# Performance work log

Hardware: AMD Instinct MI355X
Metric: run time of the kernel (lower is better)

Reference implementation:

```python
import jax, jax.numpy as jnp
import numpy as np

B, T, F, U, OUT_STEPS = 512, 128, 64, 1024, 24


def setup_inputs() -> dict:
    key = jax.random.key(0)
    k0, k1, k2, k3 = jax.random.split(key, 4)
    return {
        "inputs": jax.random.normal(k0, (B, T, F), jnp.float32),
        "Wx": jax.random.normal(k1, (F, 4 * U), jnp.float32) * 0.05,   # input kernel, gates [i|f|g|o]
        "Wh": jax.random.normal(k2, (U, 4 * U), jnp.float32) * 0.02,   # recurrent kernel
        "b": jnp.zeros((4 * U,), jnp.float32),
        "Wd": jax.random.normal(k3, (U, F), jnp.float32) * 0.03,       # Dense readout
        "bd": jnp.zeros((F,), jnp.float32),
    }


def _lstm_step(h, c, x, Wx, Wh, b):
    # Keras LSTMCell: gate order i, f, g(candidate), o; sigmoid recurrent act, tanh act.
    z = x @ Wx + h @ Wh + b                      # [B, 4U]
    i, f, g, o = jnp.split(z, 4, axis=-1)
    i = jax.nn.sigmoid(i)
    f = jax.nn.sigmoid(f)
    g = jnp.tanh(g)
    o = jax.nn.sigmoid(o)
    c_new = f * c + i * g
    h_new = o * jnp.tanh(c_new)
    return h_new, c_new


def reference(inputs, Wx, Wh, b, Wd, bd):
    Bq = inputs.shape[0]
    Uq = Wh.shape[0]
    h0 = jnp.zeros((Bq, Uq), inputs.dtype)
    c0 = jnp.zeros((Bq, Uq), inputs.dtype)

    # ---- warmup: run full LSTM over the input window, keep final state ----
    def warm(carry, x_t):
        h, c = carry
        h, c = _lstm_step(h, c, x_t, Wx, Wh, b)
        return (h, c), None

    (h, c), _ = jax.lax.scan(warm, (h0, c0), jnp.swapaxes(inputs, 0, 1))  # scan over time
    pred = h @ Wd + bd                            # first prediction [B, F]

    def decode(carry, _):
        h, c, p = carry
        h, c = _lstm_step(h, c, p, Wx, Wh, b)
        p = h @ Wd + bd
        return (h, c, p), p

    _, rest = jax.lax.scan(decode, (h, c, pred), None, length=OUT_STEPS - 1)
    preds = jnp.concatenate([pred[None], rest], axis=0)   # [OUT_STEPS, B, F]
    return jnp.swapaxes(preds, 0, 1)                       # [B, OUT_STEPS, F]
```

## Files before the change

kernel.cpp:

```cpp
#include <hip/hip_runtime.h>
#include <math.h>

#define Bq 512
#define Tq 128
#define Fq 64
#define Uq 1024
#define OSTEPS 24
#define NKC16 68

typedef _Float16 f16x8 __attribute__((ext_vector_type(8)));
typedef _Float16 f16x2 __attribute__((ext_vector_type(2)));
typedef float f32x16 __attribute__((ext_vector_type(16)));
typedef float f32x4 __attribute__((ext_vector_type(4)));
typedef float f32x2 __attribute__((ext_vector_type(2)));

__device__ __forceinline__ float sigmoidf_(float x) {
    return 1.0f / (1.0f + __expf(-x));
}
__device__ __forceinline__ float tanhf_(float x) {
    return 2.0f / (1.0f + __expf(-2.0f * x)) - 1.0f;
}

#define BAR() do {                                             \
    asm volatile("s_waitcnt lgkmcnt(0)" ::: "memory");         \
    __builtin_amdgcn_s_barrier();                              \
} while (0)

__global__ __launch_bounds__(256)
void pack_w(const float* __restrict__ Wh, const float* __restrict__ Wx,
            f16x8* __restrict__ BpH)
{
    long id = (long)blockIdx.x * 256 + threadIdx.x;
    int lane = (int)(id & 63);
    long rest = id >> 6;
    int kc16 = (int)(rest % NKC16);
    int gcol = (int)(rest / NKC16);
    int col = (gcol >> 5) * Uq + (gcol & 31) * 32 + (lane & 31);
    int k0 = kc16 * 16 + (lane >> 5) * 8;
    f16x8 hv;
#pragma unroll
    for (int j = 0; j < 8; ++j) {
        int k = k0 + j;
        float v = (k < Uq) ? Wh[(size_t)k * (4 * Uq) + col]
                           : Wx[(size_t)(k - Uq) * (4 * Uq) + col];
        hv[j] = (_Float16)v;
    }
    BpH[id] = hv;
}

#define STAGE_LOAD4(wl, bank) do {                                              \
    _Pragma("unroll")                                                           \
    for (int j_ = 0; j_ < 4; ++j_)                                              \
        ash[bank][j_] = *(const f16x8*)(hrow + ((wl) * 4 + j_) * 64);           \
} while (0)

#define STAGE_WRITE4(buf, bank) do {                                            \
    _Pragma("unroll")                                                           \
    for (int j_ = 0; j_ < 4; ++j_)                                              \
        As[buf][j_][smh][sslot] = ash[bank][j_];                                \
} while (0)

#define LOADB4(slot, wl) do {                                                   \
    _Pragma("unroll")                                                           \
    for (int j_ = 0; j_ < 4; ++j_) {                                            \
        Bh[slot][j_][0] = bpH0[(((wl) * 4 + j_) * 4 + kq) * 64];                \
        Bh[slot][j_][1] = bpH1[(((wl) * 4 + j_) * 4 + kq) * 64];                \
    }                                                                           \
} while (0)

#define COMPUTE4(buf, slot) do {                                                \
    _Pragma("unroll")                                                           \
    for (int j_ = 0; j_ < 4; ++j_) {                                            \
        f16x8 ah0_ = As[buf][j_][0][rdslot];                                    \
        f16x8 ah1_ = As[buf][j_][1][rdslot];                                    \
        __builtin_amdgcn_s_setprio(1);                                          \
        acc[0][0] = __builtin_amdgcn_mfma_f32_32x32x16_f16(ah0_, Bh[slot][j_][0], acc[0][0], 0, 0, 0); \
        acc[0][1] = __builtin_amdgcn_mfma_f32_32x32x16_f16(ah1_, Bh[slot][j_][0], acc[0][1], 0, 0, 0); \
        acc[1][0] = __builtin_amdgcn_mfma_f32_32x32x16_f16(ah0_, Bh[slot][j_][1], acc[1][0], 0, 0, 0); \
        acc[1][1] = __builtin_amdgcn_mfma_f32_32x32x16_f16(ah1_, Bh[slot][j_][1], acc[1][1], 0, 0, 0); \
        __builtin_amdgcn_s_setprio(0);                                          \
    }                                                                           \
} while (0)

__global__ __launch_bounds__(512, 2)
void lstm_step(const _Float16* __restrict__ h_in,
               const float* __restrict__ xsrc,
               long xstride,
               const f16x8* __restrict__ BpH,
               const float* __restrict__ bias,
               _Float16* __restrict__ h_out,
               float* __restrict__ c_st)
{
    __shared__ __align__(16) char smem[73728];
    f16x8 (*As)[4][2][256] = (f16x8 (*)[4][2][256])smem;
    f16x8 (*xbuf)[256] = (f16x8 (*)[256])(smem + 65536);
    float (*zsd)[4][32][36] = (float (*)[4][32][36])smem;

    const int tid = threadIdx.x;
    const int l   = tid & 63;
    const int w   = tid >> 6;
    const int gp  = w & 1;
    const int kq  = w >> 1;
    const int bm  = (int)blockIdx.x >> 5;
    const int bu  = (int)blockIdx.x & 31;
    const int row0 = bm * 64;

    const int srow = tid >> 3;
    const int kg8  = tid & 7;
    const int smh  = srow >> 5;
    const int sr31 = srow & 31;
    const int sslot = sr31 * 8 + (kg8 ^ (sr31 & 7));

    const int rdslot = (l & 31) * 8 + ((kq * 2 + (l >> 5)) ^ (l & 7));

    const f16x8* bpH0 = BpH + ((size_t)((gp * 2 + 0) * 32 + bu) * NKC16) * 64 + l;
    const f16x8* bpH1 = BpH + ((size_t)((gp * 2 + 1) * 32 + bu) * NKC16) * 64 + l;
    const _Float16* hrow = h_in + (size_t)(row0 + srow) * Uq + kg8 * 8;
    const float*    xrow = xsrc + (size_t)(row0 + srow) * xstride + kg8 * 8;

    f32x16 acc[2][2];
#pragma unroll
    for (int i = 0; i < 16; ++i) {
        acc[0][0][i] = 0.0f; acc[0][1][i] = 0.0f;
        acc[1][0][i] = 0.0f; acc[1][1][i] = 0.0f;
    }

    f16x8 Bh[2][4][2];
    f16x8 Bx[2];
    f16x8 ash[2][4];

    {
        f32x4 v0_ = *(const f32x4*)xrow;
        f32x4 v1_ = *(const f32x4*)(xrow + 4);
        f16x8 hv_;
#pragma unroll
        for (int j_ = 0; j_ < 4; ++j_) {
            hv_[j_]     = (_Float16)v0_[j_];
            hv_[4 + j_] = (_Float16)v1_[j_];
        }
        xbuf[smh][sslot] = hv_;
    }
    Bx[0] = bpH0[(64 + kq) * 64];
    Bx[1] = bpH1[(64 + kq) * 64];
    STAGE_LOAD4(0, 0);
    STAGE_LOAD4(1, 1);
    LOADB4(0, 0);
    STAGE_WRITE4(0, 0);
    BAR();

    LOADB4(1, 1);
    STAGE_LOAD4(2, 0);
    STAGE_WRITE4(1, 1);
    COMPUTE4(0, 0);
    BAR();
    LOADB4(0, 2);
    STAGE_LOAD4(3, 1);
    STAGE_WRITE4(0, 0);
    COMPUTE4(1, 1);
    BAR();
    LOADB4(1, 3);
    STAGE_WRITE4(1, 1);
    COMPUTE4(0, 0);
    BAR();
    COMPUTE4(1, 1);
    {
        f16x8 ah0_ = xbuf[0][rdslot];
        f16x8 ah1_ = xbuf[1][rdslot];
        acc[0][0] = __builtin_amdgcn_mfma_f32_32x32x16_f16(ah0_, Bx[0], acc[0][0], 0, 0, 0);
        acc[0][1] = __builtin_amdgcn_mfma_f32_32x32x16_f16(ah1_, Bx[0], acc[0][1], 0, 0, 0);
        acc[1][0] = __builtin_amdgcn_mfma_f32_32x32x16_f16(ah0_, Bx[1], acc[1][0], 0, 0, 0);
        acc[1][1] = __builtin_amdgcn_mfma_f32_32x32x16_f16(ah1_, Bx[1], acc[1][1], 0, 0, 0);
    }
    BAR();

#pragma unroll
    for (int mh = 0; mh < 2; ++mh) {
#pragma unroll
        for (int g2 = 0; g2 < 2; ++g2)
#pragma unroll
            for (int r = 0; r < 16; ++r) {
                int rowi = (r & 3) + 8 * (r >> 2) + 4 * (l >> 5);
                zsd[kq][gp * 2 + g2][rowi][l & 31] = acc[g2][mh][r];
            }
        BAR();
        {
            const int row = tid >> 4;
            const int uu  = (tid & 15) * 2;
            const int grow = row0 + mh * 32 + row;
            const int gu   = bu * 32 + uu;
            const size_t gidx = (size_t)grow * Uq + gu;
            float z[4][2];
#pragma unroll
            for (int g = 0; g < 4; ++g) {
#pragma unroll
                for (int j = 0; j < 2; ++j)
                    z[g][j] = zsd[0][g][row][uu + j] + zsd[1][g][row][uu + j]
                            + zsd[2][g][row][uu + j] + zsd[3][g][row][uu + j];
            }
            f32x2 cv = *(const f32x2*)(c_st + gidx);
            f16x2 hh;
#pragma unroll
            for (int j = 0; j < 2; ++j) {
                float vi = sigmoidf_(z[0][j] + bias[0 * Uq + gu + j]);
                float vf = sigmoidf_(z[1][j] + bias[1 * Uq + gu + j]);
                float vg = tanhf_  (z[2][j] + bias[2 * Uq + gu + j]);
                float vo = sigmoidf_(z[3][j] + bias[3 * Uq + gu + j]);
                float cn = vf * cv[j] + vi * vg;
                cv[j] = cn;
                hh[j] = (_Float16)(vo * tanhf_(cn));
            }
            *(f32x2*)(c_st + gidx) = cv;
            *(f16x2*)(h_out + gidx) = hh;
        }
        if (mh == 0) BAR();
    }
}

__global__ __launch_bounds__(256)
void readout(const _Float16* __restrict__ h, const float* __restrict__ Wd,
             const float* __restrict__ bd, float* __restrict__ p,
             float* __restrict__ out, int step)
{
    __shared__ float red[2][4][64];
    const int t = threadIdx.x;
    const int f = t & 63, kq = t >> 6;
    const int r0 = blockIdx.x * 2;
    float s0 = 0.0f, s1 = 0.0f;
    const _Float16* h0 = h + (size_t)r0 * Uq + kq * 256;
    const float* wp = Wd + (size_t)kq * 256 * Fq + f;
#pragma unroll 4
    for (int i = 0; i < 32; ++i) {
        f16x8 ah = *(const f16x8*)(h0 + i * 8);
        f16x8 bh = *(const f16x8*)(h0 + Uq + i * 8);
#pragma unroll
        for (int j = 0; j < 8; ++j) {
            float wv = wp[(size_t)(i * 8 + j) * Fq];
            s0 = fmaf((float)ah[j], wv, s0);
            s1 = fmaf((float)bh[j], wv, s1);
        }
    }
    red[0][kq][f] = s0;
    red[1][kq][f] = s1;
    __syncthreads();
    if (t < 128) {
        int rr = t >> 6, ff = t & 63;
        float s = red[rr][0][ff] + red[rr][1][ff] + red[rr][2][ff] + red[rr][3][ff] + bd[ff];
        p[(size_t)(r0 + rr) * Fq + ff] = s;
        out[((size_t)(r0 + rr) * OSTEPS + step) * Fq + ff] = s;
    }
}

__global__ void zero_ws(f32x4* __restrict__ a, int n) {
    int i = blockIdx.x * 256 + threadIdx.x;
    f32x4 z = {0.0f, 0.0f, 0.0f, 0.0f};
    if (i < n) a[i] = z;
}

extern "C" void kernel_launch(void* const* d_in, const int* in_sizes, int n_in,
                              void* d_out, int out_size, void* d_ws, size_t ws_size,
                              hipStream_t stream) {
    const float* inputs = (const float*)d_in[0];
    const float* Wx     = (const float*)d_in[1];
    const float* Wh     = (const float*)d_in[2];
    const float* b      = (const float*)d_in[3];
    const float* Wd     = (const float*)d_in[4];
    const float* bd     = (const float*)d_in[5];
    float* out = (float*)d_out;

    float* ws = (float*)d_ws;
    float* c_st = ws;
    _Float16* H0 = (_Float16*)(ws + Bq * Uq);
    _Float16* H1 = H0 + Bq * Uq;
    float* p = (float*)(H1 + Bq * Uq);
    f16x8* BpH = (f16x8*)(p + Bq * Fq);

    pack_w<<<2176, 256, 0, stream>>>(Wh, Wx, BpH);
    zero_ws<<<768, 256, 0, stream>>>((f32x4*)ws, 196608);

    _Float16 *h_c = H0, *h_n = H1;
    for (int t = 0; t < Tq; ++t) {
        lstm_step<<<256, 512, 0, stream>>>(h_c, inputs + (size_t)t * Fq, (long)Tq * Fq,
                                           BpH, b, h_n, c_st);
        _Float16* tmp = h_c; h_c = h_n; h_n = tmp;
    }
    readout<<<Bq / 2, 256, 0, stream>>>(h_c, Wd, bd, p, out, 0);
    for (int s = 1; s < OSTEPS; ++s) {
        lstm_step<<<256, 512, 0, stream>>>(h_c, p, (long)Fq, BpH, b, h_n, c_st);
        _Float16* tmp = h_c; h_c = h_n; h_n = tmp;
        readout<<<Bq / 2, 256, 0, stream>>>(h_c, Wd, bd, p, out, s);
    }
}
```

Before: 1.786 ms.

## Fold dense readout into recurrent weights for decode and batch readouts

After: 1.696 ms. -5.0%, faster.

```diff
diff --git a/kernel.cpp b/kernel.cpp
--- a/kernel.cpp
+++ b/kernel.cpp
@@ -6,7 +6,9 @@
 #define Fq 64
 #define Uq 1024
 #define OSTEPS 24
-#define NKC16 68
+#define NKC_W 68
+#define NKC_D 64
+#define SLOT ((size_t)Bq * Uq)
 
 typedef _Float16 f16x8 __attribute__((ext_vector_type(8)));
 typedef _Float16 f16x2 __attribute__((ext_vector_type(2)));
@@ -33,8 +35,8 @@
     long id = (long)blockIdx.x * 256 + threadIdx.x;
     int lane = (int)(id & 63);
     long rest = id >> 6;
-    int kc16 = (int)(rest % NKC16);
-    int gcol = (int)(rest / NKC16);
+    int kc16 = (int)(rest % NKC_W);
+    int gcol = (int)(rest / NKC_W);
     int col = (gcol >> 5) * Uq + (gcol & 31) * 32 + (lane & 31);
     int k0 = kc16 * 16 + (lane >> 5) * 8;
     f16x8 hv;
@@ -46,6 +48,65 @@
         hv[j] = (_Float16)v;
     }
     BpH[id] = hv;
+}
+
+__global__ __launch_bounds__(256)
+void wcomb_kernel(const float* __restrict__ Wh, const float* __restrict__ Wd,
+                  const float* __restrict__ Wx, float* __restrict__ Wtmp)
+{
+    __shared__ float WdL[8][64];
+    const int tid = threadIdx.x;
+    const int kb = (int)blockIdx.x >> 4;
+    const int cb = (int)blockIdx.x & 15;
+    const int k0 = kb * 8;
+    const int col = cb * 256 + tid;
+    {
+        int i0 = tid, i1 = tid + 256;
+        WdL[i0 >> 6][i0 & 63] = Wd[(size_t)(k0 + (i0 >> 6)) * Fq + (i0 & 63)];
+        WdL[i1 >> 6][i1 & 63] = Wd[(size_t)(k0 + (i1 >> 6)) * Fq + (i1 & 63)];
+    }
+    __syncthreads();
+    float acc[8];
+#pragma unroll
+    for (int kk = 0; kk < 8; ++kk)
+        acc[kk] = Wh[(size_t)(k0 + kk) * (4 * Uq) + col];
+    for (int f = 0; f < 64; ++f) {
+        float wx = Wx[(size_t)f * (4 * Uq) + col];
+#pragma unroll
+        for (int kk = 0; kk < 8; ++kk)
+            acc[kk] = fmaf(WdL[kk][f], wx, acc[kk]);
+    }
+#pragma unroll
+    for (int kk = 0; kk < 8; ++kk)
+        Wtmp[(size_t)(k0 + kk) * (4 * Uq) + col] = acc[kk];
+}
+
+__global__ __launch_bounds__(256)
+void bias2_kernel(const float* __restrict__ b, const float* __restrict__ bd,
+                  const float* __restrict__ Wx, float* __restrict__ b2)
+{
+    const int col = (int)blockIdx.x * 256 + threadIdx.x;
+    float acc = b[col];
+    for (int f = 0; f < 64; ++f)
+        acc = fmaf(bd[f], Wx[(size_t)f * (4 * Uq) + col], acc);
+    b2[col] = acc;
+}
+
+__global__ __launch_bounds__(256)
+void pack_wc(const float* __restrict__ Wtmp, f16x8* __restrict__ BpD)
+{
+    long id = (long)blockIdx.x * 256 + threadIdx.x;
+    int lane = (int)(id & 63);
+    long rest = id >> 6;
+    int kc16 = (int)(rest % NKC_D);
+    int gcol = (int)(rest / NKC_D);
+    int col = (gcol >> 5) * Uq + (gcol & 31) * 32 + (lane & 31);
+    int k0 = kc16 * 16 + (lane >> 5) * 8;
+    f16x8 hv;
+#pragma unroll
+    for (int j = 0; j < 8; ++j)
+        hv[j] = (_Float16)Wtmp[(size_t)(k0 + j) * (4 * Uq) + col];
+    BpD[id] = hv;
 }
 
 #define STAGE_LOAD4(wl, bank) do {                                              \
@@ -89,7 +150,8 @@
                const f16x8* __restrict__ BpH,
                const float* __restrict__ bias,
                _Float16* __restrict__ h_out,
-               float* __restrict__ c_st)
+               float* __restrict__ c_st,
+               int nkc, int use_x)
 {
     __shared__ __align__(16) char smem[73728];
     f16x8 (*As)[4][2][256] = (f16x8 (*)[4][2][256])smem;
@@ -113,8 +175,8 @@
 
     const int rdslot = (l & 31) * 8 + ((kq * 2 + (l >> 5)) ^ (l & 7));
 
-    const f16x8* bpH0 = BpH + ((size_t)((gp * 2 + 0) * 32 + bu) * NKC16) * 64 + l;
-    const f16x8* bpH1 = BpH + ((size_t)((gp * 2 + 1) * 32 + bu) * NKC16) * 64 + l;
+    const f16x8* bpH0 = BpH + ((size_t)((gp * 2 + 0) * 32 + bu) * nkc) * 64 + l;
+    const f16x8* bpH1 = BpH + ((size_t)((gp * 2 + 1) * 32 + bu) * nkc) * 64 + l;
     const _Float16* hrow = h_in + (size_t)(row0 + srow) * Uq + kg8 * 8;
     const float*    xrow = xsrc + (size_t)(row0 + srow) * xstride + kg8 * 8;
 
@@ -129,7 +191,7 @@
     f16x8 Bx[2];
     f16x8 ash[2][4];
 
-    {
+    if (use_x) {
         f32x4 v0_ = *(const f32x4*)xrow;
         f32x4 v1_ = *(const f32x4*)(xrow + 4);
         f16x8 hv_;
@@ -139,9 +201,9 @@
             hv_[4 + j_] = (_Float16)v1_[j_];
         }
         xbuf[smh][sslot] = hv_;
-    }
-    Bx[0] = bpH0[(64 + kq) * 64];
-    Bx[1] = bpH1[(64 + kq) * 64];
+        Bx[0] = bpH0[(64 + kq) * 64];
+        Bx[1] = bpH1[(64 + kq) * 64];
+    }
     STAGE_LOAD4(0, 0);
     STAGE_LOAD4(1, 1);
     LOADB4(0, 0);
@@ -163,7 +225,7 @@
     COMPUTE4(0, 0);
     BAR();
     COMPUTE4(1, 1);
-    {
+    if (use_x) {
         f16x8 ah0_ = xbuf[0][rdslot];
         f16x8 ah1_ = xbuf[1][rdslot];
         acc[0][0] = __builtin_amdgcn_mfma_f32_32x32x16_f16(ah0_, Bx[0], acc[0][0], 0, 0, 0);
@@ -250,6 +312,39 @@
     }
 }
 
+__global__ __launch_bounds__(256)
+void readout_all(const _Float16* __restrict__ slots, const float* __restrict__ Wd,
+                 const float* __restrict__ bd, float* __restrict__ out)
+{
+    __shared__ float red[2][4][64];
+    const int t = threadIdx.x;
+    const int f = t & 63, kq = t >> 6;
+    const int s = (int)blockIdx.x >> 8;
+    const int r0 = ((int)blockIdx.x & 255) * 2;
+    const _Float16* h0 = slots + (size_t)s * SLOT + (size_t)r0 * Uq + kq * 256;
+    float s0 = 0.0f, s1 = 0.0f;
+    const float* wp = Wd + (size_t)kq * 256 * Fq + f;
+#pragma unroll 4
+    for (int i = 0; i < 32; ++i) {
+        f16x8 ah = *(const f16x8*)(h0 + i * 8);
+        f16x8 bh = *(const f16x8*)(h0 + Uq + i * 8);
+#pragma unroll
+        for (int j = 0; j < 8; ++j) {
+            float wv = wp[(size_t)(i * 8 + j) * Fq];
+            s0 = fmaf((float)ah[j], wv, s0);
+            s1 = fmaf((float)bh[j], wv, s1);
+        }
+    }
+    red[0][kq][f] = s0;
+    red[1][kq][f] = s1;
+    __syncthreads();
+    if (t < 128) {
+        int rr = t >> 6, ff = t & 63;
+        float sum = red[rr][0][ff] + red[rr][1][ff] + red[rr][2][ff] + red[rr][3][ff] + bd[ff];
+        out[((size_t)(r0 + rr) * OSTEPS + s) * Fq + ff] = sum;
+    }
+}
+
 __global__ void zero_ws(f32x4* __restrict__ a, int n) {
     int i = blockIdx.x * 256 + threadIdx.x;
     f32x4 z = {0.0f, 0.0f, 0.0f, 0.0f};
@@ -266,27 +361,68 @@
     const float* Wd     = (const float*)d_in[4];
     const float* bd     = (const float*)d_in[5];
     float* out = (float*)d_out;
-
-    float* ws = (float*)d_ws;
-    float* c_st = ws;
-    _Float16* H0 = (_Float16*)(ws + Bq * Uq);
-    _Float16* H1 = H0 + Bq * Uq;
-    float* p = (float*)(H1 + Bq * Uq);
-    f16x8* BpH = (f16x8*)(p + Bq * Fq);
-
-    pack_w<<<2176, 256, 0, stream>>>(Wh, Wx, BpH);
-    zero_ws<<<768, 256, 0, stream>>>((f32x4*)ws, 196608);
-
-    _Float16 *h_c = H0, *h_n = H1;
-    for (int t = 0; t < Tq; ++t) {
-        lstm_step<<<256, 512, 0, stream>>>(h_c, inputs + (size_t)t * Fq, (long)Tq * Fq,
-                                           BpH, b, h_n, c_st);
-        _Float16* tmp = h_c; h_c = h_n; h_n = tmp;
-    }
-    readout<<<Bq / 2, 256, 0, stream>>>(h_c, Wd, bd, p, out, 0);
-    for (int s = 1; s < OSTEPS; ++s) {
-        lstm_step<<<256, 512, 0, stream>>>(h_c, p, (long)Fq, BpH, b, h_n, c_st);
-        _Float16* tmp = h_c; h_c = h_n; h_n = tmp;
-        readout<<<Bq / 2, 256, 0, stream>>>(h_c, Wd, bd, p, out, s);
-    }
-}
+    char* ws = (char*)d_ws;
+
+    const size_t off_slots = 2097152;
+    const size_t off_Bw    = off_slots + 25ull * 1048576;
+    const size_t off_Bd    = off_Bw + 8912896;
+    const size_t off_b2    = off_Bd + 8388608;
+    const size_t need_fold = off_b2 + 16384;
+    const int fold = (ws_size >= need_fold) ? 1 : 0;
+
+    if (fold) {
+        float*    c_st  = (float*)ws;
+        _Float16* slots = (_Float16*)(ws + off_slots);
+        f16x8*    Bw    = (f16x8*)(ws + off_Bw);
+        f16x8*    Bd    = (f16x8*)(ws + off_Bd);
+        float*    b2    = (float*)(ws + off_b2);
+        float*    Wtmp  = (float*)(ws + off_slots);
+
+        pack_w<<<2176, 256, 0, stream>>>(Wh, Wx, Bw);
+        wcomb_kernel<<<2048, 256, 0, stream>>>(Wh, Wd, Wx, Wtmp);
+        bias2_kernel<<<16, 256, 0, stream>>>(b, bd, Wx, b2);
+        pack_wc<<<2048, 256, 0, stream>>>(Wtmp, Bd);
+        zero_ws<<<768, 256, 0, stream>>>((f32x4*)ws, 196608);
+
+        _Float16* aux = slots + 24 * SLOT;
+        _Float16* hc = slots;
+        _Float16* hn = aux;
+        for (int t = 0; t < Tq; ++t) {
+            lstm_step<<<256, 512, 0, stream>>>(hc, inputs + (size_t)t * Fq,
+                                               (long)Tq * Fq, Bw, b, hn, c_st,
+                                               NKC_W, 1);
+            _Float16* tmp = hc; hc = hn; hn = tmp;
+        }
+        for (int s = 1; s < OSTEPS; ++s) {
+            lstm_step<<<256, 512, 0, stream>>>(slots + (size_t)(s - 1) * SLOT,
+                                               inputs, (long)Fq, Bd, b2,
+                                               slots + (size_t)s * SLOT, c_st,
+                                               NKC_D, 0);
+        }
+        readout_all<<<24 * 256, 256, 0, stream>>>(slots, Wd, bd, out);
+    } else {
+        float* c_st = (float*)ws;
+        _Float16* H0 = (_Float16*)(ws + 2097152);
+        _Float16* H1 = H0 + SLOT;
+        float* p = (float*)(H1 + SLOT);
+        f16x8* Bw = (f16x8*)((char*)p + Bq * Fq * 4);
+
+        pack_w<<<2176, 256, 0, stream>>>(Wh, Wx, Bw);
+        zero_ws<<<768, 256, 0, stream>>>((f32x4*)ws, 196608);
+
+        _Float16 *hc = H0, *hn = H1;
+        for (int t = 0; t < Tq; ++t) {
+            lstm_step<<<256, 512, 0, stream>>>(hc, inputs + (size_t)t * Fq,
+                                               (long)Tq * Fq, Bw, b, hn, c_st,
+                                               NKC_W, 1);
+            _Float16* tmp = hc; hc = hn; hn = tmp;
+        }
+        readout<<<Bq / 2, 256, 0, stream>>>(hc, Wd, bd, p, out, 0);
+        for (int s = 1; s < OSTEPS; ++s) {
+            lstm_step<<<256, 512, 0, stream>>>(hc, p, (long)Fq, Bw, b, hn, c_st,
+                                               NKC_W, 1);
+            _Float16* tmp = hc; hc = hn; hn = tmp;
+            readout<<<Bq / 2, 256, 0, stream>>>(hc, Wd, bd, p, out, s);
+        }
+    }
+}
```
